# Kernel tuning notes

Measured on AMD Instinct MI355X. Metric: run time of the kernel, lower is better.

## Reference

```python
import jax, jax.numpy as jnp
import numpy as np

D_MODEL, N_HEADS, D_HEAD = 1024, 16, 64
BATCH, SEQ = 4, 2048


def setup_inputs() -> dict:
    key = jax.random.key(0)
    ks = jax.random.split(key, 10)
    s = 1.0 / np.sqrt(D_MODEL)
    x = jax.random.normal(ks[0], (BATCH, SEQ, D_MODEL), dtype=jnp.float32)
    attention_mask = jax.random.randint(ks[1], (BATCH, SEQ), 0, 2).astype(jnp.bool_)
    # guarantee at least one attended key per batch row (avoid all -inf softmax)
    attention_mask = attention_mask.at[:, 0].set(True)
    def lin(k):
        kw, kb = jax.random.split(k)
        W = jax.random.uniform(kw, (D_MODEL, D_MODEL), jnp.float32, -s, s)
        b = jax.random.uniform(kb, (D_MODEL,), jnp.float32, -s, s)
        return W, b
    Wq, bq = lin(ks[2]); Wk, bk = lin(ks[3]); Wv, bv = lin(ks[4]); Wo, bo = lin(ks[5])
    return {"x": x, "attention_mask": attention_mask,
            "Wq": Wq, "bq": bq, "Wk": Wk, "bk": bk,
            "Wv": Wv, "bv": bv, "Wo": Wo, "bo": bo}


def reference(x, attention_mask, Wq, bq, Wk, bk, Wv, bv, Wo, bo):
    B, S, _ = x.shape
    def proj(W, b):  # [B,S,d_model] -> [B,S,H,Dh]
        return (x @ W + b).reshape(B, S, N_HEADS, D_HEAD)
    q = proj(Wq, bq)
    k = proj(Wk, bk)
    v = proj(Wv, bv)
    scores = jnp.einsum('bqhd,bkhd->bhqk', q, k)  # [B,H,S,S]
    add_mask = jnp.where(attention_mask, 0.0, jnp.inf)[:, None, None, :]
    # faithful order: subtract mask, THEN scale (inf survives division)
    probs = jax.nn.softmax((scores - add_mask) / jnp.sqrt(jnp.float32(D_HEAD)), axis=-1)
    attn = jnp.einsum('bhqk,bkhd->bqhd', probs, v).reshape(B, S, N_HEADS * D_HEAD)
    return attn @ Wo + bo
```

## Files before the change

### kernel.cpp

```cpp
#include <hip/hip_runtime.h>
#include <hip/hip_bf16.h>
#include <math.h>

#define BATCH 4
#define SEQ   2048
#define DM    1024
#define NH    16
#define DH    64
#define MROWS (BATCH * SEQ)

typedef unsigned short ushort_t;
typedef unsigned int   uint_t;
typedef __attribute__((ext_vector_type(8))) short  short8;
typedef __attribute__((ext_vector_type(4))) float  float4v;

#define QSCALE 0.1803368801111244f

__device__ __forceinline__ ushort_t f2bf(float v) {
    uint_t u = __float_as_uint(v);
    u += 0x7FFFu + ((u >> 16) & 1u);
    return (ushort_t)(u >> 16);
}
__device__ __forceinline__ float bf2f(ushort_t h) {
    return __uint_as_float(((uint_t)h) << 16);
}
__device__ __forceinline__ void gload_lds16(const ushort_t* g, ushort_t* lds) {
    __builtin_amdgcn_global_load_lds(
        (const __attribute__((address_space(1))) void*)g,
        (__attribute__((address_space(3))) void*)lds, 16, 0, 0);
}

__global__ __launch_bounds__(256) void conv_x(
    const float* __restrict__ src, ushort_t* __restrict__ dst, int n4)
{
    int i = blockIdx.x * 256 + threadIdx.x;
    if (i >= n4) return;
    float4 v = ((const float4*)src)[i];
    ((ushort4*)dst)[i] = make_ushort4(f2bf(v.x), f2bf(v.y), f2bf(v.z), f2bf(v.w));
}

__global__ __launch_bounds__(256) void convT_w4(
    const float* __restrict__ W0, const float* __restrict__ W1,
    const float* __restrict__ W2, const float* __restrict__ W3,
    ushort_t* __restrict__ fused, ushort_t* __restrict__ woh,
    ushort_t* __restrict__ wol)
{
    __shared__ float sT[64][65];
    const int z = blockIdx.z;
    const float* W = (z == 0) ? W0 : (z == 1) ? W1 : (z == 2) ? W2 : W3;
    ushort_t* ht = (z < 3) ? fused + (size_t)z * 1024 * 1024 : woh;
    const int n0 = blockIdx.x * 64, k0 = blockIdx.y * 64;
    const int t = threadIdx.x;
#pragma unroll
    for (int i = 0; i < 16; i++) {
        int idx = t + i * 256, r = idx >> 6, c = idx & 63;
        sT[r][c] = W[(size_t)(k0 + r) * 1024 + n0 + c];
    }
    __syncthreads();
#pragma unroll
    for (int i = 0; i < 16; i++) {
        int idx = t + i * 256, r = idx >> 6, c = idx & 63;
        float v = sT[c][r];
        ushort_t h = f2bf(v);
        ht[(size_t)(n0 + r) * 1024 + k0 + c] = h;
        if (z == 3) wol[(size_t)(n0 + r) * 1024 + k0 + c] = f2bf(v - bf2f(h));
    }
}

#define BAR()   asm volatile("s_barrier" ::: "memory")
#define LGKM0() asm volatile("s_waitcnt lgkmcnt(0)" ::: "memory")
#define VMW2()  asm volatile("s_waitcnt vmcnt(2)" ::: "memory")

#define STAGE_A(D, HA, KT) do {                                              \
    const ushort_t* _s = prowA + (size_t)(HA) * 131072 +                     \
                         (size_t)((KT) & 15) * 64;                           \
    gload_lds16(_s,         &smem[(D) * 32768 + (HA) * 8192 + dstw]);        \
    gload_lds16(_s + 65536, &smem[(D) * 32768 + (HA) * 8192 + 4096 + dstw]); \
  } while (0)

#define STAGE_B(D, HB, KT) do {                                              \
    const ushort_t* _s = prowB + (size_t)(HB) * 131072 +                     \
                         (size_t)((KT) & 15) * 64;                           \
    gload_lds16(_s,         &smem[(D) * 32768 + 16384 + (HB) * 8192 + dstw]);\
    gload_lds16(_s + 65536, &smem[(D) * 32768 + 16384 + (HB) * 8192 + 4096 + dstw]); \
  } while (0)

#define LOAD_A(D, MQ) do {                                                   \
    const int _b = (D) * 32768 + wm * 8192 + (MQ) * 4096;                    \
    _Pragma("unroll")                                                        \
    for (int mf = 0; mf < 4; mf++) {                                         \
      av[mf][0] = *(const short8*)&smem[_b + mf * 1024 + aA0];               \
      av[mf][1] = *(const short8*)&smem[_b + mf * 1024 + aA1];               \
    }                                                                        \
  } while (0)

#define LOAD_B(D, NQ) do {                                                   \
    const int _b = (D) * 32768 + 16384 + (wn >> 1) * 8192 +                  \
                   (wn & 1) * 4096 + (NQ) * 2048;                            \
    _Pragma("unroll")                                                        \
    for (int nf = 0; nf < 2; nf++) {                                         \
      bvf[nf][0] = *(const short8*)&smem[_b + nf * 1024 + aA0];              \
      bvf[nf][1] = *(const short8*)&smem[_b + nf * 1024 + aA1];              \
    }                                                                        \
  } while (0)

#define MFMA_Q(MQ, NQ) do {                                                  \
    __builtin_amdgcn_s_setprio(1);                                           \
    _Pragma("unroll")                                                        \
    for (int kk = 0; kk < 2; kk++)                                           \
      _Pragma("unroll")                                                      \
      for (int nf = 0; nf < 2; nf++)                                         \
        _Pragma("unroll")                                                    \
        for (int mf = 0; mf < 4; mf++)                                       \
          acc[(MQ) * 4 + mf][(NQ) * 2 + nf] =                                \
              __builtin_amdgcn_mfma_f32_16x16x32_bf16(                       \
                  av[mf][kk], bvf[nf][kk],                                   \
                  acc[(MQ) * 4 + mf][(NQ) * 2 + nf], 0, 0, 0);               \
    __builtin_amdgcn_s_setprio(0);                                           \
  } while (0)

__global__ __launch_bounds__(512, 2) void gemm_qkv(
    const ushort_t* __restrict__ A, const ushort_t* __restrict__ Bt,
    const float* __restrict__ bq, const float* __restrict__ bk,
    const float* __restrict__ bv, const int* __restrict__ mask,
    ushort_t* __restrict__ Qh, ushort_t* __restrict__ Kh,
    ushort_t* __restrict__ Vt)
{
    __shared__ __align__(16) ushort_t smem[65536];
    const int t = threadIdx.x, lane = t & 63, w = t >> 6;

    int bid = blockIdx.y * 12 + blockIdx.x;
    bid = (bid & 7) * 48 + (bid >> 3);
    const int n0 = (bid % 12) * 256, m0 = (bid / 12) * 256;

    const int wm = w >> 2, wn = w & 3;
    const int lq = lane >> 4, lc = lane & 15;
    const int gl = (lane & 7) ^ ((lane >> 3) & 7);
    const int sect = n0 >> 10;
    const float* bsel = (sect == 0) ? bq : (sect == 1) ? bk : bv;
    const float scl = (sect == 0) ? QSCALE : 1.0f;

    const ushort_t* prowA = A  + (size_t)(m0 + w * 8 + (lane >> 3)) * 1024 + gl * 8;
    const ushort_t* prowB = Bt + (size_t)(n0 + w * 8 + (lane >> 3)) * 1024 + gl * 8;
    const int dstw = w * 512;

    const int aA0 = lc * 64 + ((lq ^ (lc & 7)) * 8);
    const int aA1 = lc * 64 + (((4 + lq) ^ (lc & 7)) * 8);

    float4v acc[8][4];
#pragma unroll
    for (int i = 0; i < 8; i++)
#pragma unroll
        for (int j = 0; j < 4; j++) acc[i][j] = (float4v)(0.0f);

    short8 av[4][2], bvf[2][2];

    STAGE_A(0, 0, 0); STAGE_B(0, 0, 0); STAGE_A(0, 1, 0); STAGE_B(0, 1, 0);
    STAGE_A(1, 0, 1);
    VMW2();
    BAR();

    for (int i = 0; i < 8; i++) {
        const int kt = 2 * i;
        LOAD_A(0, 0); LOAD_B(0, 0); STAGE_A(1, 1, kt + 1);
        BAR(); LGKM0(); MFMA_Q(0, 0); BAR();
        LOAD_B(0, 1); STAGE_B(1, 0, kt + 1);
        BAR(); LGKM0(); MFMA_Q(0, 1); BAR();
        LOAD_A(0, 1); STAGE_B(1, 1, kt + 1);
        BAR(); LGKM0(); MFMA_Q(1, 1); BAR();
        LOAD_B(0, 0); STAGE_A(0, 0, kt + 2);
        BAR(); LGKM0(); MFMA_Q(1, 0); VMW2(); BAR();
        LOAD_A(1, 0); LOAD_B(1, 0); STAGE_B(0, 0, kt + 2);
        BAR(); LGKM0(); MFMA_Q(0, 0); BAR();
        LOAD_B(1, 1); STAGE_A(0, 1, kt + 2);
        BAR(); LGKM0(); MFMA_Q(0, 1); BAR();
        LOAD_A(1, 1); STAGE_B(0, 1, kt + 2);
        BAR(); LGKM0(); MFMA_Q(1, 1); BAR();
        LOAD_B(1, 0); STAGE_A(1, 0, kt + 3);
        BAR(); LGKM0(); MFMA_Q(1, 0); VMW2(); BAR();
    }

#pragma unroll
    for (int nf = 0; nf < 4; nf++) {
        const int nn = (n0 + wn * 64 + nf * 16 + lc) & 1023;
        const float bvv = bsel[nn];
        const int h = nn >> 6, d = nn & 63;
#pragma unroll
        for (int mf = 0; mf < 8; mf++) {
            const int mbase = m0 + wm * 128 + mf * 16 + lq * 4;
            const int b = mbase >> 11, s0 = mbase & 2047;
            int mk[4] = {1, 1, 1, 1};
            if (sect != 0) {
                const int4 m4 = *(const int4*)&mask[b * 2048 + s0];
                mk[0] = m4.x; mk[1] = m4.y; mk[2] = m4.z; mk[3] = m4.w;
            }
            if (sect == 2) {
                ushort_t hh[4];
#pragma unroll
                for (int r = 0; r < 4; r++)
                    hh[r] = mk[r] ? f2bf(acc[mf][nf][r] + bvv) : (ushort_t)0;
                *(ushort4*)&Vt[((size_t)(b * 16 + h) * 64 + d) * 2048 + s0] =
                    make_ushort4(hh[0], hh[1], hh[2], hh[3]);
            } else {
                ushort_t* dst = (sect == 0) ? Qh : Kh;
#pragma unroll
                for (int r = 0; r < 4; r++)
                    dst[((size_t)(b * 16 + h) * 2048 + s0 + r) * 64 + d] =
                        mk[r] ? f2bf((acc[mf][nf][r] + bvv) * scl) : (ushort_t)0;
            }
        }
    }
}

#undef STAGE_A
#undef STAGE_B
#undef LOAD_A
#undef LOAD_B
#undef MFMA_Q
#undef BAR
#undef LGKM0
#undef VMW2

__global__ __launch_bounds__(256) void gemm_split3(
    const ushort_t* __restrict__ Ah, const ushort_t* __restrict__ Al,
    const ushort_t* __restrict__ Bh, const ushort_t* __restrict__ Bl,
    const float* __restrict__ bias, float* __restrict__ out)
{
    __shared__ __align__(16) ushort_t smem[16384];
    const int t = threadIdx.x, lane = t & 63, w = t >> 6;
    const int n0 = blockIdx.x * 128, m0 = blockIdx.y * 128;
    const int wm = (w >> 1) * 64, wn = (w & 1) * 64;
    const int lq = lane >> 4, lc = lane & 15;
    const int gl = (lane & 3) ^ ((lane >> 3) & 3);
    const int irow = lane >> 2;

    float4v acc[4][4];
#pragma unroll
    for (int i = 0; i < 4; i++)
#pragma unroll
        for (int j = 0; j < 4; j++) acc[i][j] = (float4v)(0.0f);

    const ushort_t* plane = (w == 0) ? Ah : (w == 1) ? Al : (w == 2) ? Bh : Bl;
    const size_t prow = (size_t)(((w < 2) ? m0 : n0) + irow) * 1024 + gl * 8;

    for (int k0 = 0; k0 < 1024; k0 += 32) {
        __syncthreads();
#pragma unroll
        for (int j = 0; j < 8; j++)
            gload_lds16(plane + prow + (size_t)j * 16384 + k0, &smem[w * 4096 + j * 512]);
        __syncthreads();

        short8 ah[4], al[4];
#pragma unroll
        for (int mt = 0; mt < 4; mt++) {
            const int r = wm + mt * 16 + lc;
            const int off = r * 32 + ((lq ^ ((r >> 1) & 3)) * 8);
            ah[mt] = *(const short8*)&smem[off];
            al[mt] = *(const short8*)&smem[4096 + off];
        }
#pragma unroll
        for (int nt = 0; nt < 4; nt++) {
            const int r = wn + nt * 16 + lc;
            const int off = r * 32 + ((lq ^ ((r >> 1) & 3)) * 8);
            short8 bh = *(const short8*)&smem[8192 + off];
            short8 bl = *(const short8*)&smem[12288 + off];
#pragma unroll
            for (int mt = 0; mt < 4; mt++) {
                acc[mt][nt] = __builtin_amdgcn_mfma_f32_16x16x32_bf16(ah[mt], bh, acc[mt][nt], 0, 0, 0);
                acc[mt][nt] = __builtin_amdgcn_mfma_f32_16x16x32_bf16(al[mt], bh, acc[mt][nt], 0, 0, 0);
                acc[mt][nt] = __builtin_amdgcn_mfma_f32_16x16x32_bf16(ah[mt], bl, acc[mt][nt], 0, 0, 0);
            }
        }
    }

#pragma unroll
    for (int nt = 0; nt < 4; nt++) {
        const int n = n0 + wn + nt * 16 + lc;
        const float bvv = bias[n];
#pragma unroll
        for (int mt = 0; mt < 4; mt++)
#pragma unroll
            for (int r = 0; r < 4; r++) {
                const int m = m0 + wm + mt * 16 + lq * 4 + r;
                out[(size_t)m * 1024 + n] = acc[mt][nt][r] + bvv;
            }
    }
}

__global__ __launch_bounds__(256, 4) void flash_mfma(
    const ushort_t* __restrict__ Q, const ushort_t* __restrict__ K,
    const ushort_t* __restrict__ Vt, const int* __restrict__ mask,
    ushort_t* __restrict__ Oh, ushort_t* __restrict__ Ol)
{
    __shared__ __align__(16) ushort_t smem[16384];
    const int t = threadIdx.x, lane = t & 63, w = t >> 6;
    const int q0 = blockIdx.x * 128;
    const int bh = blockIdx.y, b = bh >> 4, h = bh & 15;
    const int lq = lane >> 4, lc = lane & 15;
    const int wm = w * 32;
    const int gl = (lane & 7) ^ ((lane >> 3) & 7);
    const int lc7 = lc & 7;

    const short8 onesf = (short8)(lc == 0 ? (short)0x3F80 : (short)0);

    int cnt;
    {
        const int4* mrow = (const int4*)(mask + b * SEQ);
        const int4 a = mrow[t * 2], c = mrow[t * 2 + 1];
        cnt = (a.x == 0) + (a.y == 0) + (a.z == 0) + (a.w == 0) +
              (c.x == 0) + (c.y == 0) + (c.z == 0) + (c.w == 0);
#pragma unroll
        for (int off = 1; off < 64; off <<= 1) cnt += __shfl_xor(cnt, off);
        if (lane == 0) ((float*)&smem[8192])[w] = (float)cnt;
    }
#pragma unroll
    for (int j = 0; j < 4; j++) {
        const int i = w * 4 + j;
        gload_lds16(Q + ((size_t)bh * SEQ + q0 + i * 8 + (lane >> 3)) * 64 + gl * 8,
                    &smem[i * 512]);
    }
    __syncthreads();
    const float nmaskf = ((const float*)&smem[8192])[0] + ((const float*)&smem[8192])[1] +
                         ((const float*)&smem[8192])[2] + ((const float*)&smem[8192])[3];

    short8 aq[2][2];
#pragma unroll
    for (int mt = 0; mt < 2; mt++)
#pragma unroll
        for (int kk = 0; kk < 2; kk++) {
            const int r = wm + mt * 16 + lc;
            aq[mt][kk] = *(const short8*)&smem[r * 64 + (((kk * 4 + lq) ^ (r & 7)) * 8)];
        }

    int aK[2], aPw[4], aPr[2];
#pragma unroll
    for (int kk = 0; kk < 2; kk++) {
        aK[kk]  = lc * 64 + (((kk * 4 + lq) ^ lc7) * 8);
        aPr[kk] = wm * 64 + aK[kk];
    }
#pragma unroll
    for (int kt4 = 0; kt4 < 4; kt4++)
        aPw[kt4] = wm * 64 + lc * 64 + (((kt4 * 2 + (lq >> 1)) ^ lc7) * 8) + (lq & 1) * 4;

    const ushort_t* gsrc;
    int gstride;
    int dstbase;
    int jstride;
    if (w < 2) {
        gsrc = K + ((size_t)bh * SEQ + w * 32 + (lane >> 3)) * 64 + gl * 8;
        gstride = 64 * 64;  dstbase = 8192 + w * 2048;  jstride = 512;
    } else {
        gsrc = Vt + ((size_t)bh * 64 + (w - 2) * 32 + (lane >> 3)) * SEQ + gl * 8;
        gstride = 64;       dstbase = 12288 + (w - 2) * 2048;  jstride = 8 * 2048;
    }

    float4v O[2][4];
    float4v lacc[2];
#pragma unroll
    for (int mt = 0; mt < 2; mt++) {
#pragma unroll
        for (int nt = 0; nt < 4; nt++) O[mt][nt] = (float4v)(0.0f);
        lacc[mt] = (float4v)(0.0f);
    }

    for (int kt = 0; kt < 32; kt++) {
        __syncthreads();
#pragma unroll
        for (int j = 0; j < 4; j++)
            gload_lds16(gsrc + j * jstride, &smem[dstbase + j * 512]);
        gsrc += gstride;
        __syncthreads();

        float4v sc[4][2];
#pragma unroll
        for (int kt4 = 0; kt4 < 4; kt4++)
#pragma unroll
            for (int mt = 0; mt < 2; mt++) sc[kt4][mt] = (float4v)(0.0f);
#pragma unroll
        for (int kk = 0; kk < 2; kk++) {
#pragma unroll
            for (int kt4 = 0; kt4 < 4; kt4++) {
                short8 ak = *(const short8*)&smem[8192 + kt4 * 1024 + aK[kk]];
#pragma unroll
                for (int mt = 0; mt < 2; mt++)
                    sc[kt4][mt] = __builtin_amdgcn_mfma_f32_16x16x32_bf16(ak, aq[mt][kk], sc[kt4][mt], 0, 0, 0);
            }
        }

#pragma unroll
        for (int kt4 = 0; kt4 < 4; kt4++) {
#pragma unroll
            for (int mt = 0; mt < 2; mt++) {
                const float p0 = __builtin_amdgcn_exp2f(sc[kt4][mt][0]);
                const float p1 = __builtin_amdgcn_exp2f(sc[kt4][mt][1]);
                const float p2 = __builtin_amdgcn_exp2f(sc[kt4][mt][2]);
                const float p3 = __builtin_amdgcn_exp2f(sc[kt4][mt][3]);
                __hip_bfloat162 pk01 = __float22bfloat162_rn(make_float2(p0, p1));
                __hip_bfloat162 pk23 = __float22bfloat162_rn(make_float2(p2, p3));
                *(uint2*)&smem[mt * 1024 + aPw[kt4]] =
                    make_uint2(*(const uint_t*)&pk01, *(const uint_t*)&pk23);
            }
        }

#pragma unroll
        for (int kk = 0; kk < 2; kk++) {
            short8 ap[2];
#pragma unroll
            for (int mt = 0; mt < 2; mt++)
                ap[mt] = *(const short8*)&smem[mt * 1024 + aPr[kk]];
#pragma unroll
            for (int mt = 0; mt < 2; mt++)
                lacc[mt] = __builtin_amdgcn_mfma_f32_16x16x32_bf16(ap[mt], onesf, lacc[mt], 0, 0, 0);
#pragma unroll
            for (int nt = 0; nt < 4; nt++) {
                short8 bv = *(const short8*)&smem[12288 + nt * 1024 + aK[kk]];
#pragma unroll
                for (int mt = 0; mt < 2; mt++)
                    O[mt][nt] = __builtin_amdgcn_mfma_f32_16x16x32_bf16(ap[mt], bv, O[mt][nt], 0, 0, 0);
            }
        }
    }

#pragma unroll
    for (int mt = 0; mt < 2; mt++) {
#pragma unroll
        for (int r = 0; r < 4; r++) {
            const float lsum = __shfl(lacc[mt][r], lane & 48) - nmaskf;
            const float inv = 1.0f / lsum;
            const int srow = q0 + wm + mt * 16 + lq * 4 + r;
#pragma unroll
            for (int nt = 0; nt < 4; nt++) {
                const float v = O[mt][nt][r] * inv;
                const ushort_t hh = f2bf(v);
                const size_t idx = ((size_t)(b * SEQ + srow)) * 1024 + h * 64 + nt * 16 + lc;
                Oh[idx] = hh;
                Ol[idx] = f2bf(v - bf2f(hh));
            }
        }
    }
}

extern "C" void kernel_launch(void* const* d_in, const int* in_sizes, int n_in,
                              void* d_out, int out_size, void* d_ws, size_t ws_size,
                              hipStream_t stream) {
    const float* x    = (const float*)d_in[0];
    const int*   mask = (const int*)d_in[1];
    const float* Wq   = (const float*)d_in[2];
    const float* bq   = (const float*)d_in[3];
    const float* Wk   = (const float*)d_in[4];
    const float* bk   = (const float*)d_in[5];
    const float* Wv   = (const float*)d_in[6];
    const float* bv   = (const float*)d_in[7];
    const float* Wo   = (const float*)d_in[8];
    const float* bo   = (const float*)d_in[9];
    float* out = (float*)d_out;

    ushort_t* p = (ushort_t*)d_ws;
    const size_t PLANE  = (size_t)MROWS * DM;
    const size_t WPLANE = (size_t)DM * DM;
    ushort_t* xh  = p;  p += PLANE;
    ushort_t* wf  = p;  p += 3 * WPLANE;
    ushort_t* woh = p;  p += WPLANE;
    ushort_t* wol = p;  p += WPLANE;
    ushort_t* Qh  = p;  p += PLANE;
    ushort_t* Kh  = p;  p += PLANE;
    ushort_t* Vth = p;  p += PLANE;
    ushort_t* Ath = p;  p += PLANE;
    ushort_t* Atl = p;  p += PLANE;

    dim3 blk(256);
    hipLaunchKernelGGL(conv_x, dim3(8192), blk, 0, stream, x, xh, 2097152);
    hipLaunchKernelGGL(convT_w4, dim3(16, 16, 4), blk, 0, stream,
                       Wq, Wk, Wv, Wo, wf, woh, wol);
    hipLaunchKernelGGL(gemm_qkv, dim3(12, 32), dim3(512), 0, stream,
                       xh, wf, bq, bk, bv, mask, Qh, Kh, Vth);
    hipLaunchKernelGGL(flash_mfma, dim3(16, 64), blk, 0, stream,
                       Qh, Kh, Vth, mask, Ath, Atl);
    hipLaunchKernelGGL(gemm_split3, dim3(8, 64), blk, 0, stream,
                       Ath, Atl, woh, wol, bo, out);
}
```

Baseline: 331.6 us.

## Shrink QKV GEMM tile to 128x256 with triple-buffered LDS pipeline

```diff
diff --git a/kernel.cpp b/kernel.cpp
--- a/kernel.cpp
+++ b/kernel.cpp
@@ -69,42 +69,41 @@
 
 #define BAR()   asm volatile("s_barrier" ::: "memory")
 #define LGKM0() asm volatile("s_waitcnt lgkmcnt(0)" ::: "memory")
-#define VMW2()  asm volatile("s_waitcnt vmcnt(2)" ::: "memory")
-
-#define STAGE_A(D, HA, KT) do {                                              \
-    const ushort_t* _s = prowA + (size_t)(HA) * 131072 +                     \
-                         (size_t)((KT) & 15) * 64;                           \
-    gload_lds16(_s,         &smem[(D) * 32768 + (HA) * 8192 + dstw]);        \
-    gload_lds16(_s + 65536, &smem[(D) * 32768 + (HA) * 8192 + 4096 + dstw]); \
+#define VMW6()  asm volatile("s_waitcnt vmcnt(6)" ::: "memory")
+
+#define STAGE_A(BO, KT) do {                                                 \
+    const ushort_t* _s = prowA + (size_t)((KT) & 15) * 64;                   \
+    gload_lds16(_s,         &smem[(BO) + dstw]);                             \
+    gload_lds16(_s + 65536, &smem[(BO) + 4096 + dstw]);                      \
   } while (0)
 
-#define STAGE_B(D, HB, KT) do {                                              \
-    const ushort_t* _s = prowB + (size_t)(HB) * 131072 +                     \
-                         (size_t)((KT) & 15) * 64;                           \
-    gload_lds16(_s,         &smem[(D) * 32768 + 16384 + (HB) * 8192 + dstw]);\
-    gload_lds16(_s + 65536, &smem[(D) * 32768 + 16384 + (HB) * 8192 + 4096 + dstw]); \
+#define STAGE_B(BO, KT) do {                                                 \
+    const ushort_t* _s = prowB + (size_t)((KT) & 15) * 64;                   \
+    gload_lds16(_s,          &smem[(BO) + 8192  + dstw]);                    \
+    gload_lds16(_s + 65536,  &smem[(BO) + 12288 + dstw]);                    \
+    gload_lds16(_s + 131072, &smem[(BO) + 16384 + dstw]);                    \
+    gload_lds16(_s + 196608, &smem[(BO) + 20480 + dstw]);                    \
   } while (0)
 
-#define LOAD_A(D, MQ) do {                                                   \
-    const int _b = (D) * 32768 + wm * 8192 + (MQ) * 4096;                    \
+#define LOAD_AV(BO) do {                                                     \
     _Pragma("unroll")                                                        \
     for (int mf = 0; mf < 4; mf++) {                                         \
-      av[mf][0] = *(const short8*)&smem[_b + mf * 1024 + aA0];               \
-      av[mf][1] = *(const short8*)&smem[_b + mf * 1024 + aA1];               \
+      av[mf][0] = *(const short8*)&smem[(BO) + aAm + mf * 1024 + aA0];       \
+      av[mf][1] = *(const short8*)&smem[(BO) + aAm + mf * 1024 + aA1];       \
     }                                                                        \
   } while (0)
 
-#define LOAD_B(D, NQ) do {                                                   \
-    const int _b = (D) * 32768 + 16384 + (wn >> 1) * 8192 +                  \
-                   (wn & 1) * 4096 + (NQ) * 2048;                            \
+#define LOAD_BV(BO, NQ) do {                                                 \
     _Pragma("unroll")                                                        \
     for (int nf = 0; nf < 2; nf++) {                                         \
-      bvf[nf][0] = *(const short8*)&smem[_b + nf * 1024 + aA0];              \
-      bvf[nf][1] = *(const short8*)&smem[_b + nf * 1024 + aA1];              \
+      bvf[nf][0] = *(const short8*)&smem[(BO) + 8192 + aBn + (NQ) * 2048 +   \
+                                         nf * 1024 + aA0];                   \
+      bvf[nf][1] = *(const short8*)&smem[(BO) + 8192 + aBn + (NQ) * 2048 +   \
+                                         nf * 1024 + aA1];                   \
     }                                                                        \
   } while (0)
 
-#define MFMA_Q(MQ, NQ) do {                                                  \
+#define MFMA_H(NQ) do {                                                      \
     __builtin_amdgcn_s_setprio(1);                                           \
     _Pragma("unroll")                                                        \
     for (int kk = 0; kk < 2; kk++)                                           \
@@ -112,10 +111,9 @@
       for (int nf = 0; nf < 2; nf++)                                         \
         _Pragma("unroll")                                                    \
         for (int mf = 0; mf < 4; mf++)                                       \
-          acc[(MQ) * 4 + mf][(NQ) * 2 + nf] =                                \
+          acc[mf][(NQ) * 2 + nf] =                                           \
               __builtin_amdgcn_mfma_f32_16x16x32_bf16(                       \
-                  av[mf][kk], bvf[nf][kk],                                   \
-                  acc[(MQ) * 4 + mf][(NQ) * 2 + nf], 0, 0, 0);               \
+                  av[mf][kk], bvf[nf][kk], acc[mf][(NQ) * 2 + nf], 0, 0, 0); \
     __builtin_amdgcn_s_setprio(0);                                           \
   } while (0)
 
@@ -126,12 +124,12 @@
     ushort_t* __restrict__ Qh, ushort_t* __restrict__ Kh,
     ushort_t* __restrict__ Vt)
 {
-    __shared__ __align__(16) ushort_t smem[65536];
+    __shared__ __align__(16) ushort_t smem[73728];
     const int t = threadIdx.x, lane = t & 63, w = t >> 6;
 
     int bid = blockIdx.y * 12 + blockIdx.x;
-    bid = (bid & 7) * 48 + (bid >> 3);
-    const int n0 = (bid % 12) * 256, m0 = (bid / 12) * 256;
+    bid = (bid & 7) * 96 + (bid >> 3);
+    const int n0 = (bid % 12) * 256, m0 = (bid / 12) * 128;
 
     const int wm = w >> 2, wn = w & 3;
     const int lq = lane >> 4, lc = lane & 15;
@@ -146,38 +144,29 @@
 
     const int aA0 = lc * 64 + ((lq ^ (lc & 7)) * 8);
     const int aA1 = lc * 64 + (((4 + lq) ^ (lc & 7)) * 8);
-
-    float4v acc[8][4];
-#pragma unroll
-    for (int i = 0; i < 8; i++)
+    const int aAm = wm * 4096;
+    const int aBn = wn * 4096;
+
+    float4v acc[4][4];
+#pragma unroll
+    for (int i = 0; i < 4; i++)
 #pragma unroll
         for (int j = 0; j < 4; j++) acc[i][j] = (float4v)(0.0f);
 
     short8 av[4][2], bvf[2][2];
 
-    STAGE_A(0, 0, 0); STAGE_B(0, 0, 0); STAGE_A(0, 1, 0); STAGE_B(0, 1, 0);
-    STAGE_A(1, 0, 1);
-    VMW2();
+    STAGE_A(0, 0); STAGE_B(0, 0); STAGE_A(24576, 1); STAGE_B(24576, 1);
+    VMW6();
     BAR();
 
-    for (int i = 0; i < 8; i++) {
-        const int kt = 2 * i;
-        LOAD_A(0, 0); LOAD_B(0, 0); STAGE_A(1, 1, kt + 1);
-        BAR(); LGKM0(); MFMA_Q(0, 0); BAR();
-        LOAD_B(0, 1); STAGE_B(1, 0, kt + 1);
-        BAR(); LGKM0(); MFMA_Q(0, 1); BAR();
-        LOAD_A(0, 1); STAGE_B(1, 1, kt + 1);
-        BAR(); LGKM0(); MFMA_Q(1, 1); BAR();
-        LOAD_B(0, 0); STAGE_A(0, 0, kt + 2);
-        BAR(); LGKM0(); MFMA_Q(1, 0); VMW2(); BAR();
-        LOAD_A(1, 0); LOAD_B(1, 0); STAGE_B(0, 0, kt + 2);
-        BAR(); LGKM0(); MFMA_Q(0, 0); BAR();
-        LOAD_B(1, 1); STAGE_A(0, 1, kt + 2);
-        BAR(); LGKM0(); MFMA_Q(0, 1); BAR();
-        LOAD_A(1, 1); STAGE_B(0, 1, kt + 2);
-        BAR(); LGKM0(); MFMA_Q(1, 1); BAR();
-        LOAD_B(1, 0); STAGE_A(1, 0, kt + 3);
-        BAR(); LGKM0(); MFMA_Q(1, 0); VMW2(); BAR();
+    int bc = 0, bs = 49152;
+    for (int kt = 0; kt < 16; kt++) {
+        LOAD_AV(bc); LOAD_BV(bc, 0); STAGE_A(bs, kt + 2);
+        BAR(); LGKM0(); MFMA_H(0); BAR();
+        LOAD_BV(bc, 1); STAGE_B(bs, kt + 2);
+        BAR(); LGKM0(); MFMA_H(1); VMW6(); BAR();
+        bc = (bc == 49152) ? 0 : bc + 24576;
+        bs = (bs == 49152) ? 0 : bs + 24576;
     }
 
 #pragma unroll
@@ -186,8 +175,8 @@
         const float bvv = bsel[nn];
         const int h = nn >> 6, d = nn & 63;
 #pragma unroll
-        for (int mf = 0; mf < 8; mf++) {
-            const int mbase = m0 + wm * 128 + mf * 16 + lq * 4;
+        for (int mf = 0; mf < 4; mf++) {
+            const int mbase = m0 + wm * 64 + mf * 16 + lq * 4;
             const int b = mbase >> 11, s0 = mbase & 2047;
             int mk[4] = {1, 1, 1, 1};
             if (sect != 0) {
@@ -214,12 +203,12 @@
 
 #undef STAGE_A
 #undef STAGE_B
-#undef LOAD_A
-#undef LOAD_B
-#undef MFMA_Q
+#undef LOAD_AV
+#undef LOAD_BV
+#undef MFMA_H
 #undef BAR
 #undef LGKM0
-#undef VMW2
+#undef VMW6
 
 __global__ __launch_bounds__(256) void gemm_split3(
     const ushort_t* __restrict__ Ah, const ushort_t* __restrict__ Al,
@@ -472,7 +461,7 @@
     hipLaunchKernelGGL(conv_x, dim3(8192), blk, 0, stream, x, xh, 2097152);
     hipLaunchKernelGGL(convT_w4, dim3(16, 16, 4), blk, 0, stream,
                        Wq, Wk, Wv, Wo, wf, woh, wol);
-    hipLaunchKernelGGL(gemm_qkv, dim3(12, 32), dim3(512), 0, stream,
+    hipLaunchKernelGGL(gemm_qkv, dim3(12, 64), dim3(512), 0, stream,
                        xh, wf, bq, bk, bv, mask, Qh, Kh, Vth);
     hipLaunchKernelGGL(flash_mfma, dim3(16, 64), blk, 0, stream,
                        Qh, Kh, Vth, mask, Ath, Atl);
```

Result: no change. 333.3 us (+0.5%).
